# Kernel optimization log

Measured on AMD Instinct MI355X. Metric: run time of the kernel, lower is better.

The kernel has to match this reference:

```python
import jax, jax.numpy as jnp
import numpy as np


def setup_inputs() -> dict:
    key = jax.random.key(0)
    ks = jax.random.split(key, 4)
    B, H, W, C = 4, 64, 64, 256
    d = C // 8
    x = jax.random.normal(ks[0], (B, H, W, C), dtype=jnp.float32)
    wq = jax.random.normal(ks[1], (C, d), dtype=jnp.float32) * (1.0 / np.sqrt(C))
    wk = jax.random.normal(ks[2], (C, d), dtype=jnp.float32) * (1.0 / np.sqrt(C))
    wv = jax.random.normal(ks[3], (C, C), dtype=jnp.float32) * (1.0 / np.sqrt(C))
    bq = jnp.zeros((d,), dtype=jnp.float32)
    bk = jnp.zeros((d,), dtype=jnp.float32)
    bv = jnp.zeros((C,), dtype=jnp.float32)
    return {"x": x, "wq": wq, "bq": bq, "wk": wk, "bk": bk, "wv": wv, "bv": bv}


def reference(x, wq, bq, wk, bk, wv, bv):
    # x: [B, H, W, C] (channels-last, as in Keras Conv2D default)
    B, H, W, C = x.shape
    N = H * W
    xf = x.reshape(B, N, C)                      # 1x1 conv == per-pixel matmul
    q = xf @ wq + bq                             # [B, N, C//8]
    k = xf @ wk + bk                             # [B, N, C//8]
    v = xf @ wv + bv                             # [B, N, C]
    # NOTE: original module applies NO 1/sqrt(d) scaling.
    attn = jax.nn.softmax(jnp.einsum('bnd,bmd->bnm', q, k), axis=-1)  # [B, N, N]
    out = jnp.einsum('bnm,bmc->bnc', attn, v)    # [B, N, C]
    return out.reshape(B, H, W, C) + x
```

## Files before the change

### kernel.cpp

```cpp
#include <hip/hip_runtime.h>
#include <stdint.h>

typedef _Float16 f16;
typedef f16 half8 __attribute__((ext_vector_type(8)));
typedef f16 half4 __attribute__((ext_vector_type(4)));
typedef float floatx4 __attribute__((ext_vector_type(4)));

#define MFMA_F16(A, B, Cc) __builtin_amdgcn_mfma_f32_16x16x32_f16((A), (B), (Cc), 0, 0, 0)

static constexpr int NB  = 4;
static constexpr int NN  = 4096;
static constexpr int NC  = 256;
static constexpr int ND  = 32;
static constexpr int PIX = NB * NN;
static constexpr int NS  = 4;
static constexpr int KS  = NN / NS;

__device__ f16 g_WbT[320 * 256];
__device__ f16 g_Qh[(size_t)PIX * ND];
__device__ f16 g_Kh[(size_t)PIX * ND];
__device__ f16 g_VbT[(size_t)NB * NC * NN];
__device__ f16 g_Of[(size_t)NS * PIX * NC];
__device__ float g_m[NS * PIX];
__device__ float g_l[NS * PIX];

__device__ inline void gl2lds16(const f16* g, f16* l) {
  __builtin_amdgcn_global_load_lds(
      (const __attribute__((address_space(1))) void*)g,
      (__attribute__((address_space(3))) void*)l, 16, 0, 0);
}

__global__ __launch_bounds__(256) void prep_weights(const float* __restrict__ wq,
                                                    const float* __restrict__ wk,
                                                    const float* __restrict__ wv) {
  const int tid = blockIdx.x * 256 + threadIdx.x;
  if (tid >= 320 * 256) return;
  const int j = tid >> 8;
  const int k = tid & 255;
  float v;
  if (j < 32)      v = wq[k * 32 + j];
  else if (j < 64) v = wk[k * 32 + (j - 32)];
  else             v = wv[k * 256 + (j - 64)];
  g_WbT[j * 256 + k] = (f16)v;
}

__global__ __launch_bounds__(256) void proj_qkv(const float* __restrict__ x,
                                                const float* __restrict__ bq,
                                                const float* __restrict__ bk,
                                                const float* __restrict__ bv) {
  __shared__ f16 xs[64 * 32];
  __shared__ f16 wsT[320 * 32];
  __shared__ f16 vt[256 * 64];

  const int tid  = threadIdx.x;
  const int lane = tid & 63;
  const int wid  = tid >> 6;
  const int qd   = lane >> 4;
  const int c16  = lane & 15;
  const int p0   = blockIdx.x * 64;
  const floatx4 zero4 = {0.f, 0.f, 0.f, 0.f};

  floatx4 acc[20];
#pragma unroll
  for (int i = 0; i < 20; ++i) acc[i] = zero4;

  for (int kk = 0; kk < 256; kk += 32) {
    {
      const int r = tid >> 2, g = tid & 3;
      const floatx4* s4 = (const floatx4*)(x + (size_t)(p0 + r) * NC + kk + g * 8);
      const floatx4 xa = s4[0], xb = s4[1];
      half8 h;
      h[0] = (f16)xa[0]; h[1] = (f16)xa[1]; h[2] = (f16)xa[2]; h[3] = (f16)xa[3];
      h[4] = (f16)xb[0]; h[5] = (f16)xb[1]; h[6] = (f16)xb[2]; h[7] = (f16)xb[3];
      *(half8*)&xs[r * 32 + g * 8] = h;
    }
#pragma unroll
    for (int i = 0; i < 10; ++i) {
      const int cid = tid + 256 * i;
      const int j = cid >> 3, m = cid & 7;
      *(half4*)&wsT[j * 32 + m * 4] = *(const half4*)&g_WbT[j * 256 + kk + m * 4];
    }
    __syncthreads();
    const half8 a = *(const half8*)&xs[(wid * 16 + c16) * 32 + qd * 8];
#pragma unroll
    for (int nt = 0; nt < 20; ++nt) {
      const half8 bfr = *(const half8*)&wsT[(nt * 16 + c16) * 32 + qd * 8];
      acc[nt] = MFMA_F16(a, bfr, acc[nt]);
    }
    __syncthreads();
  }

#pragma unroll
  for (int nt = 0; nt < 20; ++nt) {
    const int j = nt * 16 + c16;
    const float bias = (j < 32) ? bq[j] : (j < 64) ? bk[j - 32] : bv[j - 64];
#pragma unroll
    for (int r = 0; r < 4; ++r) {
      const int rl = wid * 16 + qd * 4 + r;
      const int p  = p0 + rl;
      const float val = acc[nt][r] + bias;
      if (j < 32) {
        g_Qh[(size_t)p * ND + j] = (f16)(val * 1.44269504f);
      } else if (j < 64) {
        g_Kh[(size_t)p * ND + (j - 32)] = (f16)val;
      } else {
        vt[(j - 64) * 64 + rl] = (f16)val;
      }
    }
  }
  __syncthreads();
  const int b  = p0 >> 12;
  const int n0 = p0 & (NN - 1);
#pragma unroll
  for (int i = 0; i < 16; ++i) {
    const int cid = tid + 256 * i;
    const int c = cid >> 4, m = cid & 15;
    *(half4*)(g_VbT + ((size_t)(b * NC + c)) * NN + n0 + m * 4) =
        *(const half4*)&vt[c * 64 + m * 4];
  }
}

__global__ __launch_bounds__(256, 2) void attn_split(void) {
  __shared__ f16 vsT[2][256 * 64];
  __shared__ f16 ps[4][2][16 * 64];

  const int tid  = threadIdx.x;
  const int lane = tid & 63;
  const int wid  = tid >> 6;
  const int qd   = lane >> 4;
  const int c16  = lane & 15;

  const int wgid = blockIdx.x;
  const int xcd  = wgid & 7;
  const int rem  = wgid >> 3;
  const int xblk = rem & 31;
  const int ghi  = rem >> 5;
  const int g_bs = xcd | (ghi << 3);
  const int b    = g_bs >> 2;
  const int s    = g_bs & 3;
  const int q0   = xblk * 128 + wid * 32;

  const int sx7  = c16 & 7;
  const floatx4 zero4 = {0.f, 0.f, 0.f, 0.f};

  const int vrow = wid * 64 + (lane >> 3);
  const int vchk = (lane & 7) ^ ((lane >> 3) & 7);
  const f16* vlane = g_VbT + ((size_t)(b * NC + vrow)) * NN + vchk * 8;

  half8 qf[2];
#pragma unroll
  for (int g = 0; g < 2; ++g)
    qf[g] = *(const half8*)(g_Qh + ((size_t)(b * NN + q0 + g * 16 + c16)) * ND + qd * 8);

  floatx4 acc[2][16];
#pragma unroll
  for (int g = 0; g < 2; ++g)
#pragma unroll
    for (int i = 0; i < 16; ++i) acc[g][i] = zero4;
  float m_i[2] = {-1e30f, -1e30f};
  float l_p[2] = {0.f, 0.f};

  const int kbeg = s * KS, kend = (s + 1) * KS;

  {
    f16* vdst = &vsT[0][(size_t)wid * 4096];
#pragma unroll
    for (int i = 0; i < 8; ++i)
      gl2lds16(vlane + kbeg + i * 8 * NN, vdst + i * 512);
  }
  half8 kreg[4];
#pragma unroll
  for (int a = 0; a < 4; ++a)
    kreg[a] = *(const half8*)(g_Kh + ((size_t)(b * NN + kbeg + a * 16 + c16)) * ND + qd * 8);

  for (int k0 = kbeg; k0 < kend; k0 += 64) {
    const int buf = (k0 >> 6) & 1;

    __builtin_amdgcn_s_setprio(1);
    floatx4 st[2][4];
#pragma unroll
    for (int g = 0; g < 2; ++g)
#pragma unroll
      for (int a = 0; a < 4; ++a) st[g][a] = MFMA_F16(kreg[a], qf[g], zero4);
    __builtin_amdgcn_s_setprio(0);

    float tm[2];
#pragma unroll
    for (int g = 0; g < 2; ++g) {
      float t0 = fmaxf(fmaxf(st[g][0][0], st[g][0][1]), fmaxf(st[g][0][2], st[g][0][3]));
      float t1 = fmaxf(fmaxf(st[g][1][0], st[g][1][1]), fmaxf(st[g][1][2], st[g][1][3]));
      float t2 = fmaxf(fmaxf(st[g][2][0], st[g][2][1]), fmaxf(st[g][2][2], st[g][2][3]));
      float t3 = fmaxf(fmaxf(st[g][3][0], st[g][3][1]), fmaxf(st[g][3][2], st[g][3][3]));
      tm[g] = fmaxf(fmaxf(t0, t1), fmaxf(t2, t3));
    }
    if (__any(tm[0] > m_i[0] || tm[1] > m_i[1])) {
#pragma unroll
      for (int g = 0; g < 2; ++g) {
        float tr = tm[g];
        tr = fmaxf(tr, __shfl_xor(tr, 16));
        tr = fmaxf(tr, __shfl_xor(tr, 32));
        const float m_new = (tr > m_i[g]) ? tr + 5.0f : m_i[g];
        const float alpha = exp2f(m_i[g] - m_new);
        m_i[g] = m_new;
        l_p[g] *= alpha;
        float a4[4];
#pragma unroll
        for (int r = 0; r < 4; ++r) a4[r] = __shfl(alpha, qd * 4 + r);
#pragma unroll
        for (int ct = 0; ct < 16; ++ct)
#pragma unroll
          for (int r = 0; r < 4; ++r) acc[g][ct][r] *= a4[r];
      }
    }

#pragma unroll
    for (int g = 0; g < 2; ++g) {
      float ts = 0.f;
#pragma unroll
      for (int a = 0; a < 4; ++a) {
        half4 h;
#pragma unroll
        for (int r = 0; r < 4; ++r) {
          const float p = exp2f(st[g][a][r] - m_i[g]);
          ts += p;
          h[r] = (f16)p;
        }
        const int pc = ((a * 2 + (qd >> 1)) ^ sx7) * 8 + (qd & 1) * 4;
        *(half4*)&ps[wid][g][c16 * 64 + pc] = h;
      }
      l_p[g] += ts;
    }

    __syncthreads();

    const int k0n = (k0 + 64 < kend) ? (k0 + 64) : kbeg;
    half8 knew[4];
#pragma unroll
    for (int a = 0; a < 4; ++a)
      knew[a] = *(const half8*)(g_Kh + ((size_t)(b * NN + k0n + a * 16 + c16)) * ND + qd * 8);

    half8 pa[2][2];
#pragma unroll
    for (int g = 0; g < 2; ++g)
#pragma unroll
      for (int kh = 0; kh < 2; ++kh)
        pa[g][kh] = *(const half8*)&ps[wid][g][c16 * 64 + ((kh * 4 + qd) ^ sx7) * 8];
    __builtin_amdgcn_s_setprio(1);
#pragma unroll
    for (int ct = 0; ct < 16; ++ct) {
#pragma unroll
      for (int kh = 0; kh < 2; ++kh) {
        const half8 bfr =
            *(const half8*)&vsT[buf][(ct * 16 + c16) * 64 + ((kh * 4 + qd) ^ sx7) * 8];
        acc[0][ct] = MFMA_F16(pa[0][kh], bfr, acc[0][ct]);
        acc[1][ct] = MFMA_F16(pa[1][kh], bfr, acc[1][ct]);
      }
    }
    __builtin_amdgcn_s_setprio(0);

    if (k0 + 64 < kend) {
      f16* vdst = &vsT[buf ^ 1][(size_t)wid * 4096];
#pragma unroll
      for (int i = 0; i < 8; ++i)
        gl2lds16(vlane + (k0 + 64) + i * 8 * NN, vdst + i * 512);
    }
#pragma unroll
    for (int a = 0; a < 4; ++a) kreg[a] = knew[a];
  }

#pragma unroll
  for (int g = 0; g < 2; ++g) {
    float l = l_p[g];
    l += __shfl_xor(l, 16);
    l += __shfl_xor(l, 32);
    if (qd == 0) {
      const int row = b * NN + q0 + g * 16 + c16;
      g_m[s * PIX + row] = m_i[g];
      g_l[s * PIX + row] = l;
    }
    float linv[4];
#pragma unroll
    for (int r = 0; r < 4; ++r) linv[r] = 1.0f / __shfl(l, qd * 4 + r);
#pragma unroll
    for (int ct = 0; ct < 16; ++ct)
#pragma unroll
      for (int r = 0; r < 4; ++r) {
        const int qrow = q0 + g * 16 + qd * 4 + r;
        const int c = ct * 16 + c16;
        g_Of[((size_t)(s * PIX + b * NN + qrow)) * NC + c] = (f16)(acc[g][ct][r] * linv[r]);
      }
  }
}

__global__ __launch_bounds__(256) void combine(const float* __restrict__ x,
                                               float* __restrict__ out) {
  const int tid  = threadIdx.x;
  const int lane = tid & 63;
  const int wid  = tid >> 6;
  const int row  = blockIdx.x * 4 + wid;
  const int c    = lane * 4;

  float m[NS], l[NS], M = -1e30f;
#pragma unroll
  for (int s = 0; s < NS; ++s) {
    m[s] = g_m[s * PIX + row];
    l[s] = g_l[s * PIX + row];
    M = fmaxf(M, m[s]);
  }
  float w[NS], den = 0.f;
#pragma unroll
  for (int s = 0; s < NS; ++s) { w[s] = l[s] * exp2f(m[s] - M); den += w[s]; }
  const float inv = 1.0f / den;

  float a0 = 0.f, a1 = 0.f, a2 = 0.f, a3 = 0.f;
#pragma unroll
  for (int s = 0; s < NS; ++s) {
    const half4 h = *(const half4*)&g_Of[((size_t)(s * PIX + row)) * NC + c];
    const float ws = w[s] * inv;
    a0 += ws * (float)h[0];
    a1 += ws * (float)h[1];
    a2 += ws * (float)h[2];
    a3 += ws * (float)h[3];
  }
  const floatx4 xv = *(const floatx4*)&x[(size_t)row * NC + c];
  floatx4 o;
  o[0] = a0 + xv[0]; o[1] = a1 + xv[1]; o[2] = a2 + xv[2]; o[3] = a3 + xv[3];
  *(floatx4*)&out[(size_t)row * NC + c] = o;
}

extern "C" void kernel_launch(void* const* d_in, const int* in_sizes, int n_in,
                              void* d_out, int out_size, void* d_ws, size_t ws_size,
                              hipStream_t stream) {
  (void)in_sizes; (void)n_in; (void)d_ws; (void)ws_size; (void)out_size;
  const float* x  = (const float*)d_in[0];
  const float* wq = (const float*)d_in[1];
  const float* bq = (const float*)d_in[2];
  const float* wk = (const float*)d_in[3];
  const float* bk = (const float*)d_in[4];
  const float* wv = (const float*)d_in[5];
  const float* bv = (const float*)d_in[6];
  float* out = (float*)d_out;

  hipLaunchKernelGGL(prep_weights, dim3(320), dim3(256), 0, stream, wq, wk, wv);
  hipLaunchKernelGGL(proj_qkv, dim3(256), dim3(256), 0, stream, x, bq, bk, bv);
  hipLaunchKernelGGL(attn_split, dim3(512), dim3(256), 0, stream);
  hipLaunchKernelGGL(combine, dim3(PIX / 4), dim3(256), 0, stream, x, out);
}
```

Baseline: 165.5 us.

## Software-pipeline QK^T of the next key tile with PV of the current tile

Restructures the attention loop so the QK^T scores and softmax for key tile t+1 are computed while the PV MFMAs for tile t run. P tiles, V staging and K register prefetch are each shifted one stage ahead, and the deferred accumulator rescale is applied after the PV product. A peeled prologue sets the first running max directly from the first tile, and a peeled epilogue handles the last tile. The key-tile order is also rotated per block, to spread memory access, and max reductions use three-input max. Together these aim to hide softmax latency and global load latency, at the cost of more live registers and more complex synchronisation.

```diff
diff --git a/kernel.cpp b/kernel.cpp
--- a/kernel.cpp
+++ b/kernel.cpp
@@ -28,6 +28,10 @@
   __builtin_amdgcn_global_load_lds(
       (const __attribute__((address_space(1))) void*)g,
       (__attribute__((address_space(3))) void*)l, 16, 0, 0);
+}
+
+__device__ inline float max3f(float a, float b, float c) {
+  return fmaxf(fmaxf(a, b), c);
 }
 
 __global__ __launch_bounds__(256) void prep_weights(const float* __restrict__ wq,
@@ -139,6 +143,7 @@
   const int b    = g_bs >> 2;
   const int s    = g_bs & 3;
   const int q0   = xblk * 128 + wid * 32;
+  const int ph8  = (rem & 1) * 8;
 
   const int sx7  = c16 & 7;
   const floatx4 zero4 = {0.f, 0.f, 0.f, 0.f};
@@ -147,6 +152,24 @@
   const int vchk = (lane & 7) ^ ((lane >> 3) & 7);
   const f16* vlane = g_VbT + ((size_t)(b * NC + vrow)) * NN + vchk * 8;
 
+  const int kbeg = s * KS;
+  constexpr int NT = KS / 64;
+
+  auto k_of = [&](int t) { return kbeg + ((t + ph8) & (NT - 1)) * 64; };
+  auto stage = [&](int kt, int bu) {
+    f16* vdst = &vsT[bu][(size_t)wid * 4096];
+#pragma unroll
+    for (int i = 0; i < 8; ++i)
+      gl2lds16(vlane + kt + i * 8 * NN, vdst + i * 512);
+  };
+
+  half8 kreg[4];
+  auto kload = [&](int kt) {
+#pragma unroll
+    for (int a = 0; a < 4; ++a)
+      kreg[a] = *(const half8*)(g_Kh + ((size_t)(b * NN + kt + a * 16 + c16)) * ND + qd * 8);
+  };
+
   half8 qf[2];
 #pragma unroll
   for (int g = 0; g < 2; ++g)
@@ -160,40 +183,78 @@
   float m_i[2] = {-1e30f, -1e30f};
   float l_p[2] = {0.f, 0.f};
 
-  const int kbeg = s * KS, kend = (s + 1) * KS;
-
+  kload(k_of(0));
+  stage(k_of(0), 0);
   {
-    f16* vdst = &vsT[0][(size_t)wid * 4096];
-#pragma unroll
-    for (int i = 0; i < 8; ++i)
-      gl2lds16(vlane + kbeg + i * 8 * NN, vdst + i * 512);
-  }
-  half8 kreg[4];
-#pragma unroll
-  for (int a = 0; a < 4; ++a)
-    kreg[a] = *(const half8*)(g_Kh + ((size_t)(b * NN + kbeg + a * 16 + c16)) * ND + qd * 8);
-
-  for (int k0 = kbeg; k0 < kend; k0 += 64) {
-    const int buf = (k0 >> 6) & 1;
-
-    __builtin_amdgcn_s_setprio(1);
     floatx4 st[2][4];
 #pragma unroll
     for (int g = 0; g < 2; ++g)
 #pragma unroll
       for (int a = 0; a < 4; ++a) st[g][a] = MFMA_F16(kreg[a], qf[g], zero4);
-    __builtin_amdgcn_s_setprio(0);
+    kload(k_of(1));
+#pragma unroll
+    for (int g = 0; g < 2; ++g) {
+      const floatx4* v = st[g];
+      float ta = max3f(v[0][0], v[0][1], v[0][2]);
+      float tb = max3f(v[0][3], v[1][0], v[1][1]);
+      float tc = max3f(v[1][2], v[1][3], v[2][0]);
+      float td = max3f(v[2][1], v[2][2], v[2][3]);
+      float te = max3f(v[3][0], v[3][1], v[3][2]);
+      float tr = fmaxf(max3f(ta, tb, tc), max3f(td, te, v[3][3]));
+      tr = fmaxf(tr, __shfl_xor(tr, 16));
+      tr = fmaxf(tr, __shfl_xor(tr, 32));
+      m_i[g] = tr + 5.0f;
+      float ts = 0.f;
+#pragma unroll
+      for (int a = 0; a < 4; ++a) {
+        half4 h;
+#pragma unroll
+        for (int r = 0; r < 4; ++r) {
+          const float p = exp2f(st[g][a][r] - m_i[g]);
+          ts += p;
+          h[r] = (f16)p;
+        }
+        const int pc = ((a * 2 + (qd >> 1)) ^ sx7) * 8 + (qd & 1) * 4;
+        *(half4*)&ps[wid][g][c16 * 64 + pc] = h;
+      }
+      l_p[g] = ts;
+    }
+  }
+
+  for (int t = 0; t < NT - 1; ++t) {
+    const int buf = t & 1;
+    __syncthreads();
+
+    half8 pa[2][2];
+#pragma unroll
+    for (int g = 0; g < 2; ++g)
+#pragma unroll
+      for (int kh = 0; kh < 2; ++kh)
+        pa[g][kh] = *(const half8*)&ps[wid][g][c16 * 64 + ((kh * 4 + qd) ^ sx7) * 8];
+
+    floatx4 st[2][4];
+#pragma unroll
+    for (int g = 0; g < 2; ++g)
+#pragma unroll
+      for (int a = 0; a < 4; ++a) st[g][a] = MFMA_F16(kreg[a], qf[g], zero4);
+
+    kload(k_of(t + 2));
+    stage(k_of(t + 1), buf ^ 1);
 
     float tm[2];
 #pragma unroll
     for (int g = 0; g < 2; ++g) {
-      float t0 = fmaxf(fmaxf(st[g][0][0], st[g][0][1]), fmaxf(st[g][0][2], st[g][0][3]));
-      float t1 = fmaxf(fmaxf(st[g][1][0], st[g][1][1]), fmaxf(st[g][1][2], st[g][1][3]));
-      float t2 = fmaxf(fmaxf(st[g][2][0], st[g][2][1]), fmaxf(st[g][2][2], st[g][2][3]));
-      float t3 = fmaxf(fmaxf(st[g][3][0], st[g][3][1]), fmaxf(st[g][3][2], st[g][3][3]));
-      tm[g] = fmaxf(fmaxf(t0, t1), fmaxf(t2, t3));
-    }
-    if (__any(tm[0] > m_i[0] || tm[1] > m_i[1])) {
+      const floatx4* v = st[g];
+      float ta = max3f(v[0][0], v[0][1], v[0][2]);
+      float tb = max3f(v[0][3], v[1][0], v[1][1]);
+      float tc = max3f(v[1][2], v[1][3], v[2][0]);
+      float td = max3f(v[2][1], v[2][2], v[2][3]);
+      float te = max3f(v[3][0], v[3][1], v[3][2]);
+      tm[g] = fmaxf(max3f(ta, tb, tc), max3f(td, te, v[3][3]));
+    }
+    const bool fire = __any(tm[0] > m_i[0] || tm[1] > m_i[1]);
+    float a4[2][4];
+    if (fire) {
 #pragma unroll
       for (int g = 0; g < 2; ++g) {
         float tr = tm[g];
@@ -203,13 +264,8 @@
         const float alpha = exp2f(m_i[g] - m_new);
         m_i[g] = m_new;
         l_p[g] *= alpha;
-        float a4[4];
-#pragma unroll
-        for (int r = 0; r < 4; ++r) a4[r] = __shfl(alpha, qd * 4 + r);
-#pragma unroll
-        for (int ct = 0; ct < 16; ++ct)
-#pragma unroll
-          for (int r = 0; r < 4; ++r) acc[g][ct][r] *= a4[r];
+#pragma unroll
+        for (int r = 0; r < 4; ++r) a4[g][r] = __shfl(alpha, qd * 4 + r);
       }
     }
 
@@ -231,20 +287,6 @@
       l_p[g] += ts;
     }
 
-    __syncthreads();
-
-    const int k0n = (k0 + 64 < kend) ? (k0 + 64) : kbeg;
-    half8 knew[4];
-#pragma unroll
-    for (int a = 0; a < 4; ++a)
-      knew[a] = *(const half8*)(g_Kh + ((size_t)(b * NN + k0n + a * 16 + c16)) * ND + qd * 8);
-
-    half8 pa[2][2];
-#pragma unroll
-    for (int g = 0; g < 2; ++g)
-#pragma unroll
-      for (int kh = 0; kh < 2; ++kh)
-        pa[g][kh] = *(const half8*)&ps[wid][g][c16 * 64 + ((kh * 4 + qd) ^ sx7) * 8];
     __builtin_amdgcn_s_setprio(1);
 #pragma unroll
     for (int ct = 0; ct < 16; ++ct) {
@@ -258,14 +300,37 @@
     }
     __builtin_amdgcn_s_setprio(0);
 
-    if (k0 + 64 < kend) {
-      f16* vdst = &vsT[buf ^ 1][(size_t)wid * 4096];
-#pragma unroll
-      for (int i = 0; i < 8; ++i)
-        gl2lds16(vlane + (k0 + 64) + i * 8 * NN, vdst + i * 512);
-    }
-#pragma unroll
-    for (int a = 0; a < 4; ++a) kreg[a] = knew[a];
+    if (fire) {
+#pragma unroll
+      for (int g = 0; g < 2; ++g)
+#pragma unroll
+        for (int ct = 0; ct < 16; ++ct)
+#pragma unroll
+          for (int r = 0; r < 4; ++r) acc[g][ct][r] *= a4[g][r];
+    }
+  }
+
+  {
+    const int buf = (NT - 1) & 1;
+    __syncthreads();
+    half8 pa[2][2];
+#pragma unroll
+    for (int g = 0; g < 2; ++g)
+#pragma unroll
+      for (int kh = 0; kh < 2; ++kh)
+        pa[g][kh] = *(const half8*)&ps[wid][g][c16 * 64 + ((kh * 4 + qd) ^ sx7) * 8];
+    __builtin_amdgcn_s_setprio(1);
+#pragma unroll
+    for (int ct = 0; ct < 16; ++ct) {
+#pragma unroll
+      for (int kh = 0; kh < 2; ++kh) {
+        const half8 bfr =
+            *(const half8*)&vsT[buf][(ct * 16 + c16) * 64 + ((kh * 4 + qd) ^ sx7) * 8];
+        acc[0][ct] = MFMA_F16(pa[0][kh], bfr, acc[0][ct]);
+        acc[1][ct] = MFMA_F16(pa[1][kh], bfr, acc[1][ct]);
+      }
+    }
+    __builtin_amdgcn_s_setprio(0);
   }
 
 #pragma unroll
```

Measured after the change: 178.5 us. +7.9%, slower.
